# Kernel tuning notes

Hardware: AMD Instinct MI355X
Metric: run time of the kernel (lower is better)

## Reference

```python
import jax, jax.numpy as jnp
import numpy as np

Q = 128


def _maxpool2(x):
    # 2x2 max pool, stride 2, NCHW
    return jax.lax.reduce_window(x, -jnp.inf, jax.lax.max,
                                 (1, 1, 2, 2), (1, 1, 2, 2), 'VALID')


def _conv(x, w, b):
    y = jax.lax.conv_general_dilated(x, w, window_strides=(1, 1), padding='VALID',
                                     dimension_numbers=('NCHW', 'OIHW', 'NCHW'))
    return y + b[None, :, None, None]


def setup_inputs() -> dict:
    key = jax.random.key(0)
    ks = jax.random.split(key, 16)
    B = 4096
    x = jax.random.normal(ks[0], (B, 1, 28, 28), dtype=jnp.float32)
    hash_idx1 = jax.random.randint(ks[1], (25,), 0, Q, dtype=jnp.int32)
    hash_idx2 = jax.random.randint(ks[2], (800,), 0, Q, dtype=jnp.int32)
    hash_idx3 = jax.random.randint(ks[3], (1024,), 0, Q, dtype=jnp.int32)
    # random +/-1 signs
    sgn1 = jnp.sign(jax.random.normal(ks[4], (25,), dtype=jnp.float32))
    sgn2 = jnp.sign(jax.random.normal(ks[5], (800,), dtype=jnp.float32))
    sgn3 = jnp.sign(jax.random.normal(ks[6], (1024,), dtype=jnp.float32))
    # compressed (sketched) parameters: one length-Q vector per output unit
    w1 = jax.random.normal(ks[7], (32, Q), dtype=jnp.float32) * 0.2
    b1 = jax.random.normal(ks[8], (32,), dtype=jnp.float32) * 0.05
    w2 = jax.random.normal(ks[9], (64, Q), dtype=jnp.float32) * 0.05
    b2 = jax.random.normal(ks[10], (64,), dtype=jnp.float32) * 0.05
    w3 = jax.random.normal(ks[11], (512, Q), dtype=jnp.float32) * 0.03
    b3 = jax.random.normal(ks[12], (512,), dtype=jnp.float32) * 0.05
    fc2_w = jax.random.normal(ks[13], (10, 512), dtype=jnp.float32) * 0.04
    fc2_b = jax.random.normal(ks[14], (10,), dtype=jnp.float32) * 0.05
    return {'x': x,
            'hash_idx1': hash_idx1, 'hash_idx2': hash_idx2, 'hash_idx3': hash_idx3,
            'sgn1': sgn1, 'sgn2': sgn2, 'sgn3': sgn3,
            'w1': w1, 'b1': b1, 'w2': w2, 'b2': b2, 'w3': w3, 'b3': b3,
            'fc2_w': fc2_w, 'fc2_b': fc2_b}


def reference(x, hash_idx1, hash_idx2, hash_idx3, sgn1, sgn2, sgn3,
              w1, b1, w2, b2, w3, b3, fc2_w, fc2_b):
    # SketchConv1: reconstruct dense weight via gather + sign flip
    wc1 = (w1[:, hash_idx1] * sgn1[None, :]).reshape(32, 1, 5, 5)
    h = jax.nn.relu(_maxpool2(_conv(x, wc1, b1)))          # (B,32,12,12)
    # SketchConv2
    wc2 = (w2[:, hash_idx2] * sgn2[None, :]).reshape(64, 32, 5, 5)
    h = jax.nn.relu(_maxpool2(_conv(h, wc2, b2)))          # (B,64,4,4)
    h = h.reshape(h.shape[0], -1)                          # (B,1024)
    # SketchLinear
    W3 = w3[:, hash_idx3] * sgn3[None, :]                  # (512,1024)
    h = jax.nn.relu(h @ W3.T + b3)                         # (B,512)
    logits = h @ fc2_w.T + fc2_b                           # (B,10)
    return jax.nn.log_softmax(logits, axis=1)
```

## Files before the change

kernel.cpp:

```cpp
#include <hip/hip_runtime.h>
#include <hip/hip_bf16.h>
#include <math.h>


typedef __attribute__((ext_vector_type(8))) short bf16x8;
typedef __attribute__((ext_vector_type(4))) float f32x4;

static __device__ inline ushort f2bfu(float v) {
    union { __hip_bfloat16 h; ushort u; } cv;
    cv.h = __float2bfloat16(v);
    return cv.u;
}

static __device__ inline float bfu2f(ushort u) {
    union { ushort u; __hip_bfloat16 h; } cv;
    cv.u = u;
    return __bfloat162float(cv.h);
}


__global__ __launch_bounds__(256)
void k_reconstruct(const float* __restrict__ w1, const float* __restrict__ w2,
                   const float* __restrict__ w3,
                   const int* __restrict__ hi1, const int* __restrict__ hi2,
                   const int* __restrict__ hi3,
                   const float* __restrict__ s1, const float* __restrict__ s2,
                   __hip_bfloat16* __restrict__ wc1f,
                   __hip_bfloat16* __restrict__ wc1s,
                   __hip_bfloat16* __restrict__ wc2f,
                   __hip_bfloat16* __restrict__ W3d,
                   int* __restrict__ seg, int* __restrict__ pos) {
    if (blockIdx.x == 232) {
        __shared__ int scnt[128];
        __shared__ int sincl[128];
        __shared__ int sseg[129];
        const int u = threadIdx.x;
        if (u < 128) scnt[u] = 0;
        __syncthreads();
        int qq[4], rk[4];
        #pragma unroll
        for (int j = 0; j < 4; ++j) {
            int k = u * 4 + j;
            qq[j] = hi3[k];
            rk[j] = atomicAdd(&scnt[qq[j]], 1);
        }
        __syncthreads();
        if (u < 128) {
            int v = scnt[u];
            #pragma unroll
            for (int d = 1; d < 64; d <<= 1) {
                int t2 = __shfl_up(v, d);
                if ((u & 63) >= d) v += t2;
            }
            sincl[u] = v;
        }
        __syncthreads();
        if (u < 128) {
            int base = (u >= 64) ? sincl[63] : 0;
            sseg[u + 1] = base + sincl[u];
        }
        if (u == 0) sseg[0] = 0;
        __syncthreads();
        #pragma unroll
        for (int j = 0; j < 4; ++j) {
            int k = u * 4 + j;
            pos[k] = sseg[qq[j]] + rk[j];
        }
        if (u < 129) seg[u] = sseg[u];
        return;
    }
    const int t = blockIdx.x * blockDim.x + threadIdx.x;
    const int f = t >> 2;
    const int j0 = (t & 3) * 2;
    if (f < 256) {
        const bool shifted = f >= 128;
        const int u = f & 127;
        const int nt = u >> 6, lane = u & 63;
        const int quad = lane >> 4, l15 = lane & 15;
        const int oc = nt * 16 + l15;
        ushort rr[2];
        #pragma unroll
        for (int jj = 0; jj < 2; ++jj) {
            int tt = quad * 8 + j0 + jj;
            int ki = (tt * 43) >> 8;
            int kj = tt - 6 * ki;
            float v = 0.f;
            if (!shifted && ki < 5 && kj < 5) {
                int fi = ki * 5 + kj;
                v = w1[oc * 128 + hi1[fi]] * s1[fi];
            } else if (shifted && ki < 5 && kj >= 1 && kj <= 5) {
                int fi = ki * 5 + (kj - 1);
                v = w1[oc * 128 + hi1[fi]] * s1[fi];
            }
            rr[jj] = f2bfu(v);
        }
        *(uint*)((ushort*)(shifted ? wc1s : wc1f) + (size_t)u * 8 + j0) =
            (uint)rr[0] | ((uint)rr[1] << 16);
    } else if (f < 6656) {
        const int u = f - 256;
        const int l15 = u & 15, quad = (u >> 4) & 3;
        const int ntA = (u >> 6) & 3, tap = u >> 8;
        const int oc = ntA * 16 + l15;
        ushort rr[2];
        #pragma unroll
        for (int jj = 0; jj < 2; ++jj) {
            int ic = quad * 8 + j0 + jj;
            int fi = ic * 25 + tap;
            rr[jj] = f2bfu(w2[oc * 128 + hi2[fi]] * s2[fi]);
        }
        *(uint*)((ushort*)wc2f + (size_t)u * 8 + j0) =
            (uint)rr[0] | ((uint)rr[1] << 16);
    } else if (f < 14848) {
        const int u = f - 6656;
        const int l15 = u & 15, quad = (u >> 4) & 3;
        const int kt = (u >> 6) & 3, ntile = u >> 8;
        const int n = ntile * 16 + l15;
        ushort rr[2];
        #pragma unroll
        for (int jj = 0; jj < 2; ++jj) {
            int k = kt * 32 + quad * 8 + j0 + jj;
            rr[jj] = f2bfu(w3[n * 128 + k]);
        }
        *(uint*)((ushort*)W3d + (size_t)u * 8 + j0) =
            (uint)rr[0] | ((uint)rr[1] << 16);
    }
}

__global__ __launch_bounds__(512, 6)
void k_conv(const float* __restrict__ x,
            const __hip_bfloat16* __restrict__ wc1f,
            const __hip_bfloat16* __restrict__ wc1s,
            const __hip_bfloat16* __restrict__ wc2f,
            const float* __restrict__ b1, const float* __restrict__ b2,
            const int* __restrict__ pos, const int* __restrict__ seg,
            const float* __restrict__ s3,
            __hip_bfloat16* __restrict__ h2) {
    __shared__ __align__(16) ushort s_xb[4 * 816];
    __shared__ __align__(16) ushort s_h1[16 * 1160];

    const int tid = threadIdx.x;
    const int b0 = blockIdx.x * 4;
    const int wave = tid >> 6, lane = tid & 63;
    const int l15 = lane & 15, quad = lane >> 4;

    {
        const float4* xg = (const float4*)(x + (size_t)b0 * 784);
        for (int i = tid; i < 784; i += 512) {
            float4 v = xg[i];
            int img = i / 196;
            int p = (i - img * 196) * 4;
            ushort* dst = &s_xb[img * 816 + p];
            dst[0] = f2bfu(v.x); dst[1] = f2bfu(v.y);
            dst[2] = f2bfu(v.z); dst[3] = f2bfu(v.w);
        }
        if (tid < 128) {
            int img = tid >> 5, k = tid & 31;
            s_xb[img * 816 + 784 + k] = 0;
        }
    }

    bf16x8 bw1[2], bw1s[2];
    float bb1[2];
    #pragma unroll
    for (int nt = 0; nt < 2; ++nt) {
        bw1[nt]  = *(const bf16x8*)((const ushort*)wc1f + (nt * 64 + lane) * 8);
        bw1s[nt] = *(const bf16x8*)((const ushort*)wc1s + (nt * 64 + lane) * 8);
        bb1[nt] = b1[nt * 16 + l15];
    }
    __syncthreads();

    {
        const int img = wave >> 1, half = wave & 1;
        const int sub = l15 & 3;
        const ushort* srcImg = s_xb + img * 816;
        int offr[4];
        #pragma unroll
        for (int r = 0; r < 4; ++r) {
            int t = quad * 8 + 2 * r;
            int row = (t * 43) >> 8;
            int col = t - 6 * row;
            offr[r] = row * 28 + col;
        }
        const int g0 = l15 >> 3, r0 = l15 & 7;
        #pragma unroll
        for (int ii = 0; ii < 18; ++ii) {
            const int i = half * 18 + ii;
            const int pb = 4 * i + (l15 >> 2);
            const int pi = (pb * 171) >> 11;
            const int pj = pb - 12 * pi;
            const int base_e = (2 * pi + (sub >> 1)) * 28 + 2 * pj;
            const ushort* p0 = srcImg + base_e;
            union { bf16x8 v; uint u[4]; } A;
            A.u[0] = *(const uint*)(p0 + offr[0]);
            A.u[1] = *(const uint*)(p0 + offr[1]);
            A.u[2] = *(const uint*)(p0 + offr[2]);
            A.u[3] = *(const uint*)(p0 + offr[3]);
            f32x4 z = {0.f, 0.f, 0.f, 0.f};
            f32x4 ce0 = __builtin_amdgcn_mfma_f32_16x16x32_bf16(A.v, bw1[0],  z, 0, 0, 0);
            f32x4 co0 = __builtin_amdgcn_mfma_f32_16x16x32_bf16(A.v, bw1s[0], z, 0, 0, 0);
            f32x4 ce1 = __builtin_amdgcn_mfma_f32_16x16x32_bf16(A.v, bw1[1],  z, 0, 0, 0);
            f32x4 co1 = __builtin_amdgcn_mfma_f32_16x16x32_bf16(A.v, bw1s[1], z, 0, 0, 0);
            const int pbo = 4 * i + quad;
            float m0 = fmaxf(fmaxf(ce0[0], co0[1]), fmaxf(ce0[2], co0[3]));
            float m1 = fmaxf(fmaxf(ce1[0], co1[1]), fmaxf(ce1[2], co1[3]));
            s_h1[(img * 4 + g0) * 1160 + pbo * 8 + r0]     = f2bfu(fmaxf(m0 + bb1[0], 0.f));
            s_h1[(img * 4 + 2 + g0) * 1160 + pbo * 8 + r0] = f2bfu(fmaxf(m1 + bb1[1], 0.f));
        }
    }
    __syncthreads();

    const int pr = wave >> 1, nh = wave & 1;
    const int sub2 = l15 & 3;
    const int ci2 = 2 * pr + (sub2 >> 1);
    const int cj2 = 2 * (l15 >> 2) + (sub2 & 1);
    const int posBase = (ci2 * 12 + cj2) * 8;

    f32x4 acc[4][2];
    float bb2[2];
    #pragma unroll
    for (int ntl = 0; ntl < 2; ++ntl) {
        bb2[ntl] = b2[(nh * 2 + ntl) * 16 + l15];
        #pragma unroll
        for (int img = 0; img < 4; ++img)
            acc[img][ntl] = (f32x4){0.f, 0.f, 0.f, 0.f};
    }

    #pragma unroll
    for (int tap = 0; tap < 25; ++tap) {
        const int ki = tap / 5, kj = tap % 5;
        const int off = (ki * 12 + kj) * 8;
        bf16x8 a[4];
        #pragma unroll
        for (int img = 0; img < 4; ++img)
            a[img] = *(const bf16x8*)&s_h1[(img * 4 + quad) * 1160 + posBase + off];
        #pragma unroll
        for (int ntl = 0; ntl < 2; ++ntl) {
            bf16x8 bf = *(const bf16x8*)((const ushort*)wc2f +
                          ((tap * 4 + nh * 2 + ntl) * 64 + lane) * 8);
            #pragma unroll
            for (int img = 0; img < 4; ++img)
                acc[img][ntl] = __builtin_amdgcn_mfma_f32_16x16x32_bf16(
                    a[img], bf, acc[img][ntl], 0, 0, 0);
        }
    }

    __syncthreads();

    ushort* s_hs = s_h1;
    {
        const int k0 = ((nh * 2 + 0) * 16 + l15) * 16 + pr * 4 + quad;
        const int k1 = ((nh * 2 + 1) * 16 + l15) * 16 + pr * 4 + quad;
        const int p0 = pos[k0], p1 = pos[k1];
        const float sg0 = s3[k0], sg1 = s3[k1];
        #pragma unroll
        for (int img = 0; img < 4; ++img) {
            f32x4 c0 = acc[img][0];
            float m0 = fmaxf(fmaxf(c0[0], c0[1]), fmaxf(c0[2], c0[3]));
            float v0 = fmaxf(m0 + bb2[0], 0.f);
            s_hs[img * 1024 + p0] = f2bfu(v0 * sg0);
            f32x4 c1 = acc[img][1];
            float m1 = fmaxf(fmaxf(c1[0], c1[1]), fmaxf(c1[2], c1[3]));
            float v1 = fmaxf(m1 + bb2[1], 0.f);
            s_hs[img * 1024 + p1] = f2bfu(v1 * sg1);
        }
    }
    __syncthreads();

    {
        const int img = tid >> 7, q = tid & 127;
        const int a0 = seg[q], n = seg[q + 1] - a0;
        const ushort* src = s_hs + img * 1024 + a0;
        float v = 0.f;
        for (int i = 0; i < n; ++i) v += bfu2f(src[i]);
        h2[(size_t)(b0 + img) * 128 + q] = __float2bfloat16(v);
    }
}

__global__ __launch_bounds__(1024)
void k_fc(const __hip_bfloat16* __restrict__ A, const __hip_bfloat16* __restrict__ W3d,
          const float* __restrict__ b3, const float* __restrict__ fc2w,
          const float* __restrict__ fc2b, float* __restrict__ out) {
    __shared__ __align__(16) ushort s_A[16 * 136];
    __shared__ float s_h3[16 * 516];

    const int tid = threadIdx.x;
    const int wave = tid >> 6, lane = tid & 63;
    const int l15 = lane & 15, quad = lane >> 4;
    const int mBase = blockIdx.x * 16;

    {
        const uint* g = (const uint*)(A + (size_t)(mBase + wave) * 128);
        *(uint*)&s_A[wave * 136 + lane * 2] = g[lane];
    }
    __syncthreads();

    f32x4 acc[2];
    acc[0] = (f32x4){0.f, 0.f, 0.f, 0.f};
    acc[1] = (f32x4){0.f, 0.f, 0.f, 0.f};

    const ushort* aP = &s_A[l15 * 136 + quad * 8];
    const ushort* bP0 = (const ushort*)W3d + ((size_t)(wave * 2)     * 4 * 64 + lane) * 8;
    const ushort* bP1 = (const ushort*)W3d + ((size_t)(wave * 2 + 1) * 4 * 64 + lane) * 8;
    #pragma unroll
    for (int kt = 0; kt < 4; ++kt) {
        bf16x8 a = *(const bf16x8*)(aP + kt * 32);
        bf16x8 bf0 = *(const bf16x8*)(bP0 + kt * 512);
        bf16x8 bf1 = *(const bf16x8*)(bP1 + kt * 512);
        acc[0] = __builtin_amdgcn_mfma_f32_16x16x32_bf16(a, bf0, acc[0], 0, 0, 0);
        acc[1] = __builtin_amdgcn_mfma_f32_16x16x32_bf16(a, bf1, acc[1], 0, 0, 0);
    }

    #pragma unroll
    for (int ntl = 0; ntl < 2; ++ntl) {
        int col = wave * 32 + ntl * 16 + l15;
        float bb = b3[col];
        #pragma unroll
        for (int r = 0; r < 4; ++r)
            s_h3[(quad * 4 + r) * 516 + col] = fmaxf(acc[ntl][r] + bb, 0.f);
    }
    __syncthreads();

    const float* hrow = &s_h3[wave * 516];
    float4 h0 = *(const float4*)&hrow[lane * 8];
    float4 h1 = *(const float4*)&hrow[lane * 8 + 4];
    float lg[10];
    #pragma unroll
    for (int c = 0; c < 10; ++c) {
        float4 w0 = *(const float4*)&fc2w[c * 512 + lane * 8];
        float4 w1 = *(const float4*)&fc2w[c * 512 + lane * 8 + 4];
        float s = h0.x * w0.x + h0.y * w0.y + h0.z * w0.z + h0.w * w0.w
                + h1.x * w1.x + h1.y * w1.y + h1.z * w1.z + h1.w * w1.w;
        s += __shfl_down(s, 32);
        s += __shfl_down(s, 16);
        s += __shfl_down(s, 8);
        s += __shfl_down(s, 4);
        s += __shfl_down(s, 2);
        s += __shfl_down(s, 1);
        lg[c] = s;
    }
    if (lane == 0) {
        float mx = -1e30f;
        #pragma unroll
        for (int c = 0; c < 10; ++c) { lg[c] += fc2b[c]; mx = fmaxf(mx, lg[c]); }
        float sum = 0.f;
        #pragma unroll
        for (int c = 0; c < 10; ++c) sum += expf(lg[c] - mx);
        float lse = mx + logf(sum);
        #pragma unroll
        for (int c = 0; c < 10; ++c)
            out[(size_t)(mBase + wave) * 10 + c] = lg[c] - lse;
    }
}

extern "C" void kernel_launch(void* const* d_in, const int* in_sizes, int n_in,
                              void* d_out, int out_size, void* d_ws, size_t ws_size,
                              hipStream_t stream) {
    const float* x    = (const float*)d_in[0];
    const int*   hi1  = (const int*)d_in[1];
    const int*   hi2  = (const int*)d_in[2];
    const int*   hi3  = (const int*)d_in[3];
    const float* s1   = (const float*)d_in[4];
    const float* s2   = (const float*)d_in[5];
    const float* s3   = (const float*)d_in[6];
    const float* w1   = (const float*)d_in[7];
    const float* b1   = (const float*)d_in[8];
    const float* w2   = (const float*)d_in[9];
    const float* b2   = (const float*)d_in[10];
    const float* w3   = (const float*)d_in[11];
    const float* b3   = (const float*)d_in[12];
    const float* fc2w = (const float*)d_in[13];
    const float* fc2b = (const float*)d_in[14];
    float* out = (float*)d_out;

    const int B = in_sizes[0] / 784;

    char* ws = (char*)d_ws;
    __hip_bfloat16* wc1f = (__hip_bfloat16*)(ws + 0);
    __hip_bfloat16* wc1s = (__hip_bfloat16*)(ws + 2048);
    __hip_bfloat16* wc2f = (__hip_bfloat16*)(ws + 4096);
    __hip_bfloat16* W3d  = (__hip_bfloat16*)(ws + 106496);
    int*            seg  = (int*)(ws + 237568);
    int*            pos  = (int*)(ws + 238592);
    __hip_bfloat16* h2   = (__hip_bfloat16*)(ws + 1155072);

    k_reconstruct<<<233, 256, 0, stream>>>(
        w1, w2, w3, hi1, hi2, hi3, s1, s2, wc1f, wc1s, wc2f, W3d, seg, pos);
    k_conv<<<B / 4, 512, 0, stream>>>(x, wc1f, wc1s, wc2f, b1, b2, pos, seg, s3, h2);
    k_fc<<<B / 16, 1024, 0, stream>>>(h2, W3d, b3, fc2w, fc2b, out);
}
```

Baseline: 128.8 us.

## Fuse FC layers and log-softmax into conv kernel, drop separate FC launch

Removes the k_fc kernel and the h2 global intermediate. k_conv now runs the 128->512 sketched linear layer on MFMA, followed by fc2 and log-softmax, for its 4 images. The goal is to save a kernel launch and the global round-trip of the activations. In exchange, only 4 of the 16 MFMA rows carry useful data, every block re-reads all of W3d from global or cache, and the conv kernel gets longer and uses more registers, which may hurt its occupancy.

Result: slower. 133.1 us (+3.4%).

```diff
diff --git a/kernel.cpp b/kernel.cpp
--- a/kernel.cpp
+++ b/kernel.cpp
@@ -131,12 +131,15 @@
             const __hip_bfloat16* __restrict__ wc1f,
             const __hip_bfloat16* __restrict__ wc1s,
             const __hip_bfloat16* __restrict__ wc2f,
+            const __hip_bfloat16* __restrict__ W3d,
             const float* __restrict__ b1, const float* __restrict__ b2,
             const int* __restrict__ pos, const int* __restrict__ seg,
-            const float* __restrict__ s3,
-            __hip_bfloat16* __restrict__ h2) {
+            const float* __restrict__ s3, const float* __restrict__ b3,
+            const float* __restrict__ fc2w, const float* __restrict__ fc2b,
+            float* __restrict__ out) {
     __shared__ __align__(16) ushort s_xb[4 * 816];
     __shared__ __align__(16) ushort s_h1[16 * 1160];
+    __shared__ float s_lg[4][12];
 
     const int tid = threadIdx.x;
     const int b0 = blockIdx.x * 4;
@@ -266,89 +269,83 @@
     }
     __syncthreads();
 
+    ushort* s_Ab = s_h1 + 4096;
     {
         const int img = tid >> 7, q = tid & 127;
         const int a0 = seg[q], n = seg[q + 1] - a0;
         const ushort* src = s_hs + img * 1024 + a0;
         float v = 0.f;
         for (int i = 0; i < n; ++i) v += bfu2f(src[i]);
-        h2[(size_t)(b0 + img) * 128 + q] = __float2bfloat16(v);
-    }
-}
-
-__global__ __launch_bounds__(1024)
-void k_fc(const __hip_bfloat16* __restrict__ A, const __hip_bfloat16* __restrict__ W3d,
-          const float* __restrict__ b3, const float* __restrict__ fc2w,
-          const float* __restrict__ fc2b, float* __restrict__ out) {
-    __shared__ __align__(16) ushort s_A[16 * 136];
-    __shared__ float s_h3[16 * 516];
-
-    const int tid = threadIdx.x;
-    const int wave = tid >> 6, lane = tid & 63;
-    const int l15 = lane & 15, quad = lane >> 4;
-    const int mBase = blockIdx.x * 16;
-
-    {
-        const uint* g = (const uint*)(A + (size_t)(mBase + wave) * 128);
-        *(uint*)&s_A[wave * 136 + lane * 2] = g[lane];
-    }
-    __syncthreads();
-
-    f32x4 acc[2];
-    acc[0] = (f32x4){0.f, 0.f, 0.f, 0.f};
-    acc[1] = (f32x4){0.f, 0.f, 0.f, 0.f};
-
-    const ushort* aP = &s_A[l15 * 136 + quad * 8];
-    const ushort* bP0 = (const ushort*)W3d + ((size_t)(wave * 2)     * 4 * 64 + lane) * 8;
-    const ushort* bP1 = (const ushort*)W3d + ((size_t)(wave * 2 + 1) * 4 * 64 + lane) * 8;
-    #pragma unroll
-    for (int kt = 0; kt < 4; ++kt) {
-        bf16x8 a = *(const bf16x8*)(aP + kt * 32);
-        bf16x8 bf0 = *(const bf16x8*)(bP0 + kt * 512);
-        bf16x8 bf1 = *(const bf16x8*)(bP1 + kt * 512);
-        acc[0] = __builtin_amdgcn_mfma_f32_16x16x32_bf16(a, bf0, acc[0], 0, 0, 0);
-        acc[1] = __builtin_amdgcn_mfma_f32_16x16x32_bf16(a, bf1, acc[1], 0, 0, 0);
-    }
-
-    #pragma unroll
-    for (int ntl = 0; ntl < 2; ++ntl) {
-        int col = wave * 32 + ntl * 16 + l15;
-        float bb = b3[col];
-        #pragma unroll
-        for (int r = 0; r < 4; ++r)
-            s_h3[(quad * 4 + r) * 516 + col] = fmaxf(acc[ntl][r] + bb, 0.f);
-    }
-    __syncthreads();
-
-    const float* hrow = &s_h3[wave * 516];
-    float4 h0 = *(const float4*)&hrow[lane * 8];
-    float4 h1 = *(const float4*)&hrow[lane * 8 + 4];
-    float lg[10];
-    #pragma unroll
-    for (int c = 0; c < 10; ++c) {
-        float4 w0 = *(const float4*)&fc2w[c * 512 + lane * 8];
-        float4 w1 = *(const float4*)&fc2w[c * 512 + lane * 8 + 4];
-        float s = h0.x * w0.x + h0.y * w0.y + h0.z * w0.z + h0.w * w0.w
-                + h1.x * w1.x + h1.y * w1.y + h1.z * w1.z + h1.w * w1.w;
-        s += __shfl_down(s, 32);
-        s += __shfl_down(s, 16);
-        s += __shfl_down(s, 8);
-        s += __shfl_down(s, 4);
-        s += __shfl_down(s, 2);
-        s += __shfl_down(s, 1);
-        lg[c] = s;
-    }
-    if (lane == 0) {
-        float mx = -1e30f;
-        #pragma unroll
-        for (int c = 0; c < 10; ++c) { lg[c] += fc2b[c]; mx = fmaxf(mx, lg[c]); }
+        s_Ab[img * 136 + q] = f2bfu(v);
+    }
+    __syncthreads();
+
+    float* s_h3 = (float*)(s_h1 + 5632);
+    {
+        f32x4 facc[4];
+        #pragma unroll
+        for (int ntl = 0; ntl < 4; ++ntl)
+            facc[ntl] = (f32x4){0.f, 0.f, 0.f, 0.f};
+        #pragma unroll
+        for (int kt = 0; kt < 4; ++kt) {
+            bf16x8 a = (bf16x8){0, 0, 0, 0, 0, 0, 0, 0};
+            if (l15 < 4)
+                a = *(const bf16x8*)&s_Ab[l15 * 136 + kt * 32 + quad * 8];
+            #pragma unroll
+            for (int ntl = 0; ntl < 4; ++ntl) {
+                bf16x8 bf = *(const bf16x8*)((const ushort*)W3d +
+                              (((wave * 4 + ntl) * 4 + kt) * 64 + lane) * 8);
+                facc[ntl] = __builtin_amdgcn_mfma_f32_16x16x32_bf16(
+                    a, bf, facc[ntl], 0, 0, 0);
+            }
+        }
+        if (quad == 0) {
+            #pragma unroll
+            for (int ntl = 0; ntl < 4; ++ntl) {
+                int col = wave * 64 + ntl * 16 + l15;
+                float bb = b3[col];
+                #pragma unroll
+                for (int r = 0; r < 4; ++r)
+                    s_h3[r * 528 + col] = fmaxf(facc[ntl][r] + bb, 0.f);
+            }
+        }
+    }
+    __syncthreads();
+
+    {
+        const int img = wave >> 1;
+        const float* hrow = &s_h3[img * 528];
+        float4 h0 = *(const float4*)&hrow[lane * 8];
+        float4 h1 = *(const float4*)&hrow[lane * 8 + 4];
+        #pragma unroll
+        for (int cc = 0; cc < 5; ++cc) {
+            int c = (wave & 1) * 5 + cc;
+            float4 w0 = *(const float4*)&fc2w[c * 512 + lane * 8];
+            float4 w1 = *(const float4*)&fc2w[c * 512 + lane * 8 + 4];
+            float s = h0.x * w0.x + h0.y * w0.y + h0.z * w0.z + h0.w * w0.w
+                    + h1.x * w1.x + h1.y * w1.y + h1.z * w1.z + h1.w * w1.w;
+            s += __shfl_down(s, 32);
+            s += __shfl_down(s, 16);
+            s += __shfl_down(s, 8);
+            s += __shfl_down(s, 4);
+            s += __shfl_down(s, 2);
+            s += __shfl_down(s, 1);
+            if (lane == 0) s_lg[img][c] = s + fc2b[c];
+        }
+    }
+    __syncthreads();
+
+    if (tid < 4) {
+        float lg[10], mx = -1e30f;
+        #pragma unroll
+        for (int c = 0; c < 10; ++c) { lg[c] = s_lg[tid][c]; mx = fmaxf(mx, lg[c]); }
         float sum = 0.f;
         #pragma unroll
         for (int c = 0; c < 10; ++c) sum += expf(lg[c] - mx);
         float lse = mx + logf(sum);
         #pragma unroll
         for (int c = 0; c < 10; ++c)
-            out[(size_t)(mBase + wave) * 10 + c] = lg[c] - lse;
+            out[(size_t)(b0 + tid) * 10 + c] = lg[c] - lse;
     }
 }
 
@@ -381,10 +378,9 @@
     __hip_bfloat16* W3d  = (__hip_bfloat16*)(ws + 106496);
     int*            seg  = (int*)(ws + 237568);
     int*            pos  = (int*)(ws + 238592);
-    __hip_bfloat16* h2   = (__hip_bfloat16*)(ws + 1155072);
 
     k_reconstruct<<<233, 256, 0, stream>>>(
         w1, w2, w3, hi1, hi2, hi3, s1, s2, wc1f, wc1s, wc2f, W3d, seg, pos);
-    k_conv<<<B / 4, 512, 0, stream>>>(x, wc1f, wc1s, wc2f, b1, b2, pos, seg, s3, h2);
-    k_fc<<<B / 16, 1024, 0, stream>>>(h2, W3d, b3, fc2w, fc2b, out);
-}
+    k_conv<<<B / 4, 512, 0, stream>>>(x, wc1f, wc1s, wc2f, W3d, b1, b2,
+                                      pos, seg, s3, b3, fc2w, fc2b, out);
+}
```
